# Performance work log

Measured on AMD Instinct MI355X. Metric: run time of the kernel, lower is better.

## Reference

```python
import jax, jax.numpy as jnp
import numpy as np

B, T, D_IN, D, KS = 8, 2048, 64, 512, 3
N_LAYERS = 6
TOP_P = 0.25


def _causal_conv(x, w, b, dil):
    # x: [B, C_in, T], w: [C_out, C_in, K] -> [B, C_out, T]
    pad = (w.shape[-1] - 1) * dil
    y = jax.lax.conv_general_dilated(
        x, w, window_strides=(1,), padding=[(pad, 0)], rhs_dilation=(dil,),
        dimension_numbers=('NCH', 'OIH', 'NCH'))
    return y + b[None, :, None]


def setup_inputs() -> dict:
    key = jax.random.key(0)
    ks = jax.random.split(key, 20)
    s = 0.02
    inp = {
        'x': jax.random.normal(ks[0], (B, T, D_IN), jnp.float32),
        # block 0 (d_in=64 -> d_model=512, dilation 1) + 1x1 residual
        'c1w0': jax.random.normal(ks[1], (D, D_IN, KS), jnp.float32) * s,
        'c1b0': jnp.zeros((D,), jnp.float32),
        'c2w0': jax.random.normal(ks[2], (D, D, KS), jnp.float32) * s,
        'c2b0': jnp.zeros((D,), jnp.float32),
        'resw': jax.random.normal(ks[3], (D, D_IN, 1), jnp.float32) * s,
        'resb': jnp.zeros((D,), jnp.float32),
        # blocks 1..5 stacked (512 -> 512, dilations 2,4,8,16,32), identity residual
        'c1w': jax.random.normal(ks[4], (N_LAYERS - 1, D, D, KS), jnp.float32) * s,
        'c1b': jnp.zeros((N_LAYERS - 1, D), jnp.float32),
        'c2w': jax.random.normal(ks[5], (N_LAYERS - 1, D, D, KS), jnp.float32) * s,
        'c2b': jnp.zeros((N_LAYERS - 1, D), jnp.float32),
        # attention projections (torch Linear: y = x @ W.T + b, W [out,in])
        'wq': jax.random.normal(ks[6], (D, D), jnp.float32) * s,
        'bq': jnp.zeros((D,), jnp.float32),
        'wk': jax.random.normal(ks[7], (D, D), jnp.float32) * s,
        'bk': jnp.zeros((D,), jnp.float32),
        'wv': jax.random.normal(ks[8], (D, D), jnp.float32) * s,
        'bv': jnp.zeros((D,), jnp.float32),
        'wp': jax.random.normal(ks[9], (D, D), jnp.float32) * s,
        'bp': jnp.zeros((D,), jnp.float32),
    }
    return inp


def _forward(x, c1w0, c1b0, c2w0, c2b0, resw, resb, c1w, c1b, c2w, c2b,
             wq, bq, wk, bk, wv, bv, wp, bp):
    gelu = lambda t: jax.nn.gelu(t, approximate=False)
    h = jnp.swapaxes(x, 1, 2)  # [B, D_IN, T]
    # block 0 with 1x1-conv residual (d_in != d_out)
    y = gelu(_causal_conv(h, c1w0, c1b0, 1))
    y = gelu(_causal_conv(y, c2w0, c2b0, 1))
    h = y + _causal_conv(h, resw, resb, 1)
    # blocks 1..5, identity residual
    for i in range(N_LAYERS - 1):
        dil = 2 ** (i + 1)
        y = gelu(_causal_conv(h, c1w[i], c1b[i], dil))
        y = gelu(_causal_conv(y, c2w[i], c2b[i], dil))
        h = y + h
    z = jnp.swapaxes(h, 1, 2)  # [B, T, D]

    # sparse top-p attention
    q = z @ wq.T + bq
    k = z @ wk.T + bk
    v = z @ wv.T + bv
    scores = jnp.einsum('bqd,bkd->bqk', q, k) / jnp.sqrt(jnp.float32(D))
    k_keep = max(1, int(TOP_P * T))
    vals, idx = jax.lax.top_k(scores, k_keep)  # [B, T, k_keep]
    neg_inf = jnp.array(-jnp.inf, scores.dtype)
    mask = jnp.full_like(scores, neg_inf)
    b_ix = jnp.arange(B)[:, None, None]
    t_ix = jnp.arange(T)[None, :, None]
    mask = mask.at[b_ix, t_ix, idx].set(vals)
    attn = jax.nn.softmax(mask, axis=-1)
    attn_out = jnp.einsum('bqk,bkd->bqd', attn, v)[:, -1, :]  # [B, D]

    return (z[:, -1, :] + attn_out) @ wp.T + bp


def reference(x, c1w0, c1b0, c2w0, c2b0, resw, resb, c1w, c1b, c2w, c2b,
              wq, bq, wk, bk, wv, bv, wp, bp):
    return _forward(x, c1w0, c1b0, c2w0, c2b0, resw, resb, c1w, c1b, c2w, c2b,
                    wq, bq, wk, bk, wv, bv, wp, bp)
```

## Files before the change

### kernel.cpp

```cpp
#include <hip/hip_runtime.h>
#include <hip/hip_bf16.h>
#include <math.h>

#define B_ 8
#define T_ 2048
#define PT_ 2112
#define DIN_ 64
#define D_ 512

typedef __attribute__((ext_vector_type(8))) short bf16x8;
typedef __attribute__((ext_vector_type(4))) float f32x4;

#define HROW(b, t) (((size_t)(b) * PT_ + 64 + (t)) * D_)

__device__ __forceinline__ float gelu_f(float x) {
    return 0.5f * x * (1.0f + erff(x * 0.70710678118654752440f));
}
__device__ __forceinline__ float bfu2f(unsigned short u) {
    union { float f; unsigned int i; } v; v.i = ((unsigned int)u) << 16; return v.f;
}
__device__ __forceinline__ unsigned short f2bf(float f) {
    unsigned int x = __float_as_uint(f);
    return (unsigned short)((x + 0x7FFFu + ((x >> 16) & 1u)) >> 16);
}
__device__ __forceinline__ void gload_lds16(const void* g, void* l) {
    __builtin_amdgcn_global_load_lds(
        (const __attribute__((address_space(1))) void*)g,
        (__attribute__((address_space(3))) void*)l, 16, 0, 0);
}

__global__ __launch_bounds__(256) void k_zeropad(unsigned short* xb,
                                                 unsigned short* bufA,
                                                 unsigned short* bufB) {
    const int NX = B_ * 64 * DIN_;
    const int NA = B_ * 64 * D_;
    int i = blockIdx.x * 256 + threadIdx.x;
    if (i < NX) {
        const int b = i / (64 * DIN_), r = i - b * (64 * DIN_);
        xb[(size_t)b * PT_ * DIN_ + r] = 0;
        return;
    }
    i -= NX;
    if (i < NA) {
        const int b = i / (64 * D_), r = i - b * (64 * D_);
        bufA[(size_t)b * PT_ * D_ + r] = 0;
        return;
    }
    i -= NA;
    if (i < NA) {
        const int b = i / (64 * D_), r = i - b * (64 * D_);
        bufB[(size_t)b * PT_ * D_ + r] = 0;
    }
}

__global__ __launch_bounds__(256) void k_xcvt(const float* __restrict__ x,
                                              unsigned short* __restrict__ xb, int n) {
    const int i = blockIdx.x * 256 + threadIdx.x;
    if (i >= n) return;
    const int b = i / (T_ * DIN_);
    const int r = i - b * (T_ * DIN_);
    xb[((size_t)b * PT_ + 64) * DIN_ + r] = f2bf(x[i]);
}

__global__ __launch_bounds__(256) void k_wcvt(const float* __restrict__ src,
                                              unsigned short* __restrict__ dst,
                                              int C_in, int KS) {
    const int n = 512 * C_in * KS;
    const size_t base = (size_t)blockIdx.y * n;
    for (int i = blockIdx.x * 256 + threadIdx.x; i < n; i += gridDim.x * 256) {
        const int ci = i % C_in;
        const int r = i / C_in;
        const int co = r & 511;
        const int tap = r >> 9;
        dst[base + i] = f2bf(src[base + ((size_t)co * C_in + ci) * KS + tap]);
    }
}

template <int KS, int MODE>
__global__ __launch_bounds__(256) void k_conv_mfma(const unsigned short* __restrict__ X,
                                                   const unsigned short* __restrict__ Wt,
                                                   const float* __restrict__ bias,
                                                   const unsigned short* R,
                                                   unsigned short* Y,
                                                   int C_in, int dil) {
    const int tid = threadIdx.x;
    const int t0 = blockIdx.x * 128;
    const int co0 = blockIdx.y * 128;
    const int b = blockIdx.z;
    const int back = (KS - 1) * dil;
    const int XWIN = 128 + back;

    __shared__ __align__(16) unsigned short sX[2][192 * 32];
    __shared__ __align__(16) unsigned short sW[2][KS * 128 * 32];

    const int lane = tid & 63;
    const int wv = tid >> 6;
    const int wco = (wv & 1) * 64;
    const int wt = (wv >> 1) * 64;
    const int tl = lane & 15;
    const int ch = lane >> 4;
    const int asl = ch * 8;

    f32x4 acc[4][4] = {};

    const unsigned short* Xb = X + ((size_t)b * PT_ + 64) * C_in;
    const int nxload = XWIN * 4;

    auto stage = [&](int buf, int ci0) {
        for (int i = tid; i < nxload; i += 256) {
            const int row = i >> 2, sl = i & 3;
            const int tg = t0 - back + row;
            gload_lds16(Xb + (size_t)tg * C_in + ci0 + sl * 8, &sX[buf][(i & ~63) * 8]);
        }
        for (int i = tid; i < KS * 512; i += 256) {
            const int tap = i >> 9;
            const int r = i & 511;
            const int row = r >> 2, sl = r & 3;
            gload_lds16(Wt + ((size_t)(tap * 512 + co0 + row)) * C_in + ci0 + sl * 8,
                        &sW[buf][(i & ~63) * 8]);
        }
    };

    const int NC = C_in >> 5;
    stage(0, 0);
    __syncthreads();
    int cur = 0;

    for (int c = 0; c < NC; ++c) {
        if (c + 1 < NC) stage(cur ^ 1, (c + 1) * 32);

#pragma unroll
        for (int tap = 0; tap < KS; ++tap) {
            bf16x8 a[4], bb[4];
#pragma unroll
            for (int m = 0; m < 4; ++m)
                a[m] = *reinterpret_cast<const bf16x8*>(&sW[cur][(tap * 128 + wco + m * 16 + tl) * 32 + asl]);
            const int tapoff = tap * dil;
#pragma unroll
            for (int n = 0; n < 4; ++n)
                bb[n] = *reinterpret_cast<const bf16x8*>(&sX[cur][(wt + n * 16 + tl + tapoff) * 32 + asl]);
#pragma unroll
            for (int m = 0; m < 4; ++m)
#pragma unroll
                for (int n = 0; n < 4; ++n)
                    acc[m][n] = __builtin_amdgcn_mfma_f32_16x16x32_bf16(a[m], bb[n], acc[m][n], 0, 0, 0);
        }
        __syncthreads();
        cur ^= 1;
    }

#pragma unroll
    for (int m = 0; m < 4; ++m) {
        const int co = co0 + wco + m * 16 + ch * 4;
        const float4 bv4 = *reinterpret_cast<const float4*>(&bias[co]);
#pragma unroll
        for (int n = 0; n < 4; ++n) {
            const int t = t0 + wt + n * 16 + tl;
            const size_t base = HROW(b, t) + co;
            float v[4];
            v[0] = acc[m][n][0] + bv4.x;
            v[1] = acc[m][n][1] + bv4.y;
            v[2] = acc[m][n][2] + bv4.z;
            v[3] = acc[m][n][3] + bv4.w;
            if (MODE >= 1) {
#pragma unroll
                for (int r = 0; r < 4; ++r) v[r] = gelu_f(v[r]);
            }
            if (MODE == 2) {
                const uint2 rr = *reinterpret_cast<const uint2*>(&R[base]);
                v[0] += bfu2f((unsigned short)(rr.x & 0xffffu));
                v[1] += bfu2f((unsigned short)(rr.x >> 16));
                v[2] += bfu2f((unsigned short)(rr.y & 0xffffu));
                v[3] += bfu2f((unsigned short)(rr.y >> 16));
            }
            uint2 o;
            o.x = (unsigned int)f2bf(v[0]) | ((unsigned int)f2bf(v[1]) << 16);
            o.y = (unsigned int)f2bf(v[2]) | ((unsigned int)f2bf(v[3]) << 16);
            *reinterpret_cast<uint2*>(&Y[base]) = o;
        }
    }
}

__global__ __launch_bounds__(256) void k_q(const unsigned short* __restrict__ h,
                                           const float* __restrict__ wq,
                                           const float* __restrict__ bq,
                                           float* __restrict__ q) {
    __shared__ float zs[B_ * D_];
    const int tid = threadIdx.x;
    for (int i = tid; i < B_ * D_; i += 256) {
        const int b = i >> 9, c = i & 511;
        zs[i] = bfu2f(h[HROW(b, T_ - 1) + c]);
    }
    __syncthreads();
    const int wvi = tid >> 6, lane = tid & 63;
    const int d = blockIdx.x * 4 + wvi;
    const float* wr = wq + (size_t)d * D_ + lane * 8;
    float w8[8];
#pragma unroll
    for (int j = 0; j < 8; ++j) w8[j] = wr[j];
    float acc[B_];
#pragma unroll
    for (int b = 0; b < B_; ++b) {
        float a = 0.0f;
#pragma unroll
        for (int j = 0; j < 8; ++j) a += w8[j] * zs[b * D_ + lane * 8 + j];
        acc[b] = a;
    }
#pragma unroll
    for (int off = 32; off; off >>= 1) {
#pragma unroll
        for (int b = 0; b < B_; ++b) acc[b] += __shfl_xor(acc[b], off);
    }
    if (lane == 0) {
#pragma unroll
        for (int b = 0; b < B_; ++b) q[b * D_ + d] = acc[b] + bq[d];
    }
}

__global__ __launch_bounds__(512) void k_qk(const float* __restrict__ q,
                                            const float* __restrict__ wk,
                                            const float* __restrict__ bk,
                                            float* __restrict__ qkvec,
                                            float* __restrict__ qbk) {
    const int b = blockIdx.y, dc = blockIdx.x;
    const int tid = threadIdx.x;
    __shared__ float qs[64];
    if (tid < 64) qs[tid] = q[b * D_ + dc * 64 + tid];
    __syncthreads();
    float acc = 0.0f;
    const float* wbase = wk + (size_t)(dc * 64) * D_ + tid;
#pragma unroll 8
    for (int d = 0; d < 64; ++d) acc += qs[d] * wbase[(size_t)d * D_];
    atomicAdd(&qkvec[b * D_ + tid], acc);
    if (tid < 64) {
        float p = qs[tid] * bk[dc * 64 + tid];
#pragma unroll
        for (int off = 32; off; off >>= 1) p += __shfl_xor(p, off);
        if (tid == 0) atomicAdd(&qbk[b], p);
    }
}

__global__ __launch_bounds__(256) void k_scores(const unsigned short* __restrict__ h,
                                                const float* __restrict__ qkvec,
                                                const float* __restrict__ qbk,
                                                float* __restrict__ scores) {
    const int b = blockIdx.y;
    const int tid = threadIdx.x;
    __shared__ float qs[D_];
    qs[tid] = qkvec[b * D_ + tid];
    qs[tid + 256] = qkvec[b * D_ + tid + 256];
    __syncthreads();
    const int wvi = tid >> 6, lane = tid & 63;
    const int t = blockIdx.x * 4 + wvi;
    const uint4 v = *reinterpret_cast<const uint4*>(h + HROW(b, t) + lane * 8);
    const unsigned int w[4] = {v.x, v.y, v.z, v.w};
    float acc = 0.0f;
#pragma unroll
    for (int j = 0; j < 4; ++j) {
        acc += bfu2f((unsigned short)(w[j] & 0xffffu)) * qs[lane * 8 + 2 * j];
        acc += bfu2f((unsigned short)(w[j] >> 16)) * qs[lane * 8 + 2 * j + 1];
    }
    for (int off = 32; off; off >>= 1) acc += __shfl_down(acc, off);
    if (lane == 0) scores[b * T_ + t] = (acc + qbk[b]) * 0.04419417382415922f;
}

__global__ __launch_bounds__(1024) void k_topk(const float* __restrict__ scores,
                                               float* __restrict__ wts) {
    const int b = blockIdx.x;
    __shared__ float s[T_];
    __shared__ float v[T_];
    __shared__ float red[16];
    __shared__ float denom_s;
    for (int i = threadIdx.x; i < T_; i += 1024) {
        const float x = scores[b * T_ + i];
        s[i] = x; v[i] = x;
    }
    __syncthreads();
    for (unsigned kk = 2; kk <= T_; kk <<= 1) {
        for (unsigned j = kk >> 1; j > 0; j >>= 1) {
            for (unsigned i = threadIdx.x; i < T_; i += 1024) {
                const unsigned ixj = i ^ j;
                if (ixj > i) {
                    const float a = v[i], c2 = v[ixj];
                    const bool asc = ((i & kk) == 0);
                    if ((a > c2) == asc) { v[i] = c2; v[ixj] = a; }
                }
            }
            __syncthreads();
        }
    }
    const float thr = v[T_ - 512];
    const float mx = v[T_ - 1];
    float part = 0.0f;
    for (int i = threadIdx.x; i < T_; i += 1024) {
        const float x = s[i];
        if (x >= thr) part += expf(x - mx);
    }
    for (int off = 32; off; off >>= 1) part += __shfl_down(part, off);
    const int lane = threadIdx.x & 63, wv_ = threadIdx.x >> 6;
    if (lane == 0) red[wv_] = part;
    __syncthreads();
    if (threadIdx.x == 0) {
        float d = 0.0f;
        for (int i = 0; i < 16; ++i) d += red[i];
        denom_s = d;
    }
    __syncthreads();
    const float inv = 1.0f / denom_s;
    for (int i = threadIdx.x; i < T_; i += 1024) {
        const float x = s[i];
        wts[b * T_ + i] = (x >= thr) ? expf(x - mx) * inv : 0.0f;
    }
}

__global__ __launch_bounds__(256) void k_zv(const unsigned short* __restrict__ h,
                                            const float* __restrict__ wts,
                                            float* __restrict__ zvb) {
    const int b = blockIdx.y;
    const int t0 = blockIdx.x * 256;
    const int tid = threadIdx.x;
    float a0 = 0.0f, a1 = 0.0f;
    for (int t = t0; t < t0 + 256; ++t) {
        const float w = wts[b * T_ + t];
        if (w != 0.0f) {
            const unsigned int v = *reinterpret_cast<const unsigned int*>(
                h + HROW(b, t) + tid * 2);
            a0 += w * bfu2f((unsigned short)(v & 0xffffu));
            a1 += w * bfu2f((unsigned short)(v >> 16));
        }
    }
    atomicAdd(&zvb[b * D_ + tid * 2], a0);
    atomicAdd(&zvb[b * D_ + tid * 2 + 1], a1);
}

__global__ __launch_bounds__(256) void k_u(const unsigned short* __restrict__ h,
                                           const float* __restrict__ zvb,
                                           const float* __restrict__ wv,
                                           const float* __restrict__ bv,
                                           float* __restrict__ u) {
    __shared__ float zs[B_ * D_];
    const int tid = threadIdx.x;
    for (int i = tid; i < B_ * D_; i += 256) zs[i] = zvb[i];
    __syncthreads();
    const int wvi = tid >> 6, lane = tid & 63;
    const int e = blockIdx.x * 4 + wvi;
    const float* wr = wv + (size_t)e * D_ + lane * 8;
    float w8[8];
#pragma unroll
    for (int j = 0; j < 8; ++j) w8[j] = wr[j];
    float acc[B_];
#pragma unroll
    for (int b = 0; b < B_; ++b) {
        float a = 0.0f;
#pragma unroll
        for (int j = 0; j < 8; ++j) a += w8[j] * zs[b * D_ + lane * 8 + j];
        acc[b] = a;
    }
#pragma unroll
    for (int off = 32; off; off >>= 1) {
#pragma unroll
        for (int b = 0; b < B_; ++b) acc[b] += __shfl_xor(acc[b], off);
    }
    if (lane == 0) {
#pragma unroll
        for (int b = 0; b < B_; ++b)
            u[b * D_ + e] = acc[b] + bv[e] + bfu2f(h[HROW(b, T_ - 1) + e]);
    }
}

__global__ __launch_bounds__(256) void k_out(const float* __restrict__ u,
                                             const float* __restrict__ wp,
                                             const float* __restrict__ bp,
                                             float* __restrict__ out) {
    __shared__ float us[B_ * D_];
    const int tid = threadIdx.x;
    for (int i = tid; i < B_ * D_; i += 256) us[i] = u[i];
    __syncthreads();
    const int wvi = tid >> 6, lane = tid & 63;
    const int d = blockIdx.x * 4 + wvi;
    const float* wr = wp + (size_t)d * D_ + lane * 8;
    float w8[8];
#pragma unroll
    for (int j = 0; j < 8; ++j) w8[j] = wr[j];
    float acc[B_];
#pragma unroll
    for (int b = 0; b < B_; ++b) {
        float a = 0.0f;
#pragma unroll
        for (int j = 0; j < 8; ++j) a += w8[j] * us[b * D_ + lane * 8 + j];
        acc[b] = a;
    }
#pragma unroll
    for (int off = 32; off; off >>= 1) {
#pragma unroll
        for (int b = 0; b < B_; ++b) acc[b] += __shfl_xor(acc[b], off);
    }
    if (lane == 0) {
#pragma unroll
        for (int b = 0; b < B_; ++b) out[b * D_ + d] = acc[b] + bp[d];
    }
}

extern "C" void kernel_launch(void* const* d_in, const int* in_sizes, int n_in,
                              void* d_out, int out_size, void* d_ws, size_t ws_size,
                              hipStream_t stream) {
    const float* x    = (const float*)d_in[0];
    const float* c1w0 = (const float*)d_in[1];
    const float* c1b0 = (const float*)d_in[2];
    const float* c2w0 = (const float*)d_in[3];
    const float* c2b0 = (const float*)d_in[4];
    const float* resw = (const float*)d_in[5];
    const float* resb = (const float*)d_in[6];
    const float* c1w  = (const float*)d_in[7];
    const float* c1b  = (const float*)d_in[8];
    const float* c2w  = (const float*)d_in[9];
    const float* c2b  = (const float*)d_in[10];
    const float* wq   = (const float*)d_in[11];
    const float* bq   = (const float*)d_in[12];
    const float* wk   = (const float*)d_in[13];
    const float* bk   = (const float*)d_in[14];
    const float* wvp  = (const float*)d_in[15];
    const float* bv   = (const float*)d_in[16];
    const float* wp   = (const float*)d_in[17];
    const float* bp   = (const float*)d_in[18];
    float* out = (float*)d_out;

    unsigned short* ws16 = (unsigned short*)d_ws;
    unsigned short* xb   = ws16;
    unsigned short* bufA = xb + (size_t)B_ * PT_ * DIN_;
    unsigned short* bufB = bufA + (size_t)B_ * PT_ * D_;
    unsigned short* wRes = bufB + (size_t)B_ * PT_ * D_;
    unsigned short* wC10 = wRes + 512 * 64;
    unsigned short* wC20 = wC10 + 3 * 512 * 64;
    unsigned short* wC1  = wC20 + 3 * 512 * 512;
    unsigned short* wC2  = wC1 + (size_t)5 * 3 * 512 * 512;
    float* fws  = (float*)(wC2 + (size_t)5 * 3 * 512 * 512);
    float* qv    = fws;
    float* qkvec = qv + B_ * D_;
    float* qbk   = qkvec + B_ * D_;
    float* zvb   = qbk + 8;
    float* uacc  = zvb + B_ * D_;
    float* sc    = uacc + B_ * D_;
    float* wts   = sc + B_ * T_;

    k_zeropad<<<dim3((B_ * 64 * (DIN_ + 2 * D_) + 255) / 256), 256, 0, stream>>>(xb, bufA, bufB);
    k_xcvt<<<dim3((B_ * T_ * DIN_ + 255) / 256), 256, 0, stream>>>(x, xb, B_ * T_ * DIN_);
    k_wcvt<<<dim3(128, 1), 256, 0, stream>>>(resw, wRes, DIN_, 1);
    k_wcvt<<<dim3(384, 1), 256, 0, stream>>>(c1w0, wC10, DIN_, 3);
    k_wcvt<<<dim3(768, 1), 256, 0, stream>>>(c2w0, wC20, D_, 3);
    k_wcvt<<<dim3(768, 5), 256, 0, stream>>>(c1w, wC1, D_, 3);
    k_wcvt<<<dim3(768, 5), 256, 0, stream>>>(c2w, wC2, D_, 3);
    hipMemsetAsync(qkvec, 0, (2 * B_ * D_ + 8) * sizeof(float), stream);

    const dim3 cgrid(T_ / 128, D_ / 128, B_);
    k_conv_mfma<1, 0><<<cgrid, 256, 0, stream>>>(xb, wRes, resb, nullptr, bufA, DIN_, 1);
    k_conv_mfma<3, 1><<<cgrid, 256, 0, stream>>>(xb, wC10, c1b0, nullptr, bufB, DIN_, 1);
    k_conv_mfma<3, 2><<<cgrid, 256, 0, stream>>>(bufB, wC20, c2b0, bufA, bufA, D_, 1);
    for (int i = 0; i < 5; ++i) {
        const int dil = 2 << i;
        k_conv_mfma<3, 1><<<cgrid, 256, 0, stream>>>(bufA, wC1 + (size_t)i * 3 * 512 * 512,
                                                     c1b + i * D_, nullptr, bufB, D_, dil);
        k_conv_mfma<3, 2><<<cgrid, 256, 0, stream>>>(bufB, wC2 + (size_t)i * 3 * 512 * 512,
                                                     c2b + i * D_, bufA, bufA, D_, dil);
    }

    k_q<<<128, 256, 0, stream>>>(bufA, wq, bq, qv);
    k_qk<<<dim3(8, 8), 512, 0, stream>>>(qv, wk, bk, qkvec, qbk);
    k_scores<<<dim3(T_ / 4, B_), 256, 0, stream>>>(bufA, qkvec, qbk, sc);
    k_topk<<<B_, 1024, 0, stream>>>(sc, wts);
    k_zv<<<dim3(T_ / 256, B_), 256, 0, stream>>>(bufA, wts, zvb);
    k_u<<<128, 256, 0, stream>>>(bufA, zvb, wvp, bv, uacc);
    k_out<<<128, 256, 0, stream>>>(uacc, wp, bp, out);
}
```

Before: 528.6 us.

## Widen conv K-chunk to 64 with XOR-swizzled LDS and deeper async prefetch

The MFMA causal-conv kernel now stages 64 input channels per chunk instead of 32. LDS rows are XOR-swizzled to avoid bank conflicts on the bf16x8 fragment reads. Two chunks are prefetched up front, with explicit vmcnt waits and raw s_barriers so that global-to-LDS loads overlap compute with fewer synchronisations per channel. The larger LDS footprint and launch_bounds(256,1) lower occupancy. The hardcoded vmcnt counts and the fixed 6-iteration X staging loop, which clamps row indices, depend on the exact load counts and window sizes.

```diff
diff --git a/kernel.cpp b/kernel.cpp
--- a/kernel.cpp
+++ b/kernel.cpp
@@ -77,21 +77,24 @@
 }
 
 template <int KS, int MODE>
-__global__ __launch_bounds__(256) void k_conv_mfma(const unsigned short* __restrict__ X,
-                                                   const unsigned short* __restrict__ Wt,
-                                                   const float* __restrict__ bias,
-                                                   const unsigned short* R,
-                                                   unsigned short* Y,
-                                                   int C_in, int dil) {
+__global__ __launch_bounds__(256, 1) void k_conv_mfma(const unsigned short* __restrict__ X,
+                                                      const unsigned short* __restrict__ Wt,
+                                                      const float* __restrict__ bias,
+                                                      const unsigned short* R,
+                                                      unsigned short* Y,
+                                                      int C_in, int dil) {
+    constexpr int XROWS = 192;
+    constexpr int WROWS = KS * 128;
+    constexpr int WSLOTS = WROWS * 8;
+
     const int tid = threadIdx.x;
     const int t0 = blockIdx.x * 128;
     const int co0 = blockIdx.y * 128;
     const int b = blockIdx.z;
     const int back = (KS - 1) * dil;
-    const int XWIN = 128 + back;
-
-    __shared__ __align__(16) unsigned short sX[2][192 * 32];
-    __shared__ __align__(16) unsigned short sW[2][KS * 128 * 32];
+
+    __shared__ __align__(16) unsigned short sX[2][XROWS * 64];
+    __shared__ __align__(16) unsigned short sW[2][WROWS * 64];
 
     const int lane = tid & 63;
     const int wv = tid >> 6;
@@ -99,54 +102,81 @@
     const int wt = (wv >> 1) * 64;
     const int tl = lane & 15;
     const int ch = lane >> 4;
-    const int asl = ch * 8;
 
     f32x4 acc[4][4] = {};
 
     const unsigned short* Xb = X + ((size_t)b * PT_ + 64) * C_in;
-    const int nxload = XWIN * 4;
 
     auto stage = [&](int buf, int ci0) {
-        for (int i = tid; i < nxload; i += 256) {
-            const int row = i >> 2, sl = i & 3;
-            const int tg = t0 - back + row;
-            gload_lds16(Xb + (size_t)tg * C_in + ci0 + sl * 8, &sX[buf][(i & ~63) * 8]);
-        }
-        for (int i = tid; i < KS * 512; i += 256) {
-            const int tap = i >> 9;
-            const int r = i & 511;
-            const int row = r >> 2, sl = r & 3;
-            gload_lds16(Wt + ((size_t)(tap * 512 + co0 + row)) * C_in + ci0 + sl * 8,
+#pragma unroll
+        for (int k = 0; k < 6; ++k) {
+            const int i = tid + k * 256;
+            const int row = i >> 3, s = i & 7;
+            int tg = t0 - back + row;
+            if (tg >= T_) tg = T_ - 1;
+            gload_lds16(Xb + (size_t)tg * C_in + ci0 + ((s ^ (row & 7)) << 3),
+                        &sX[buf][(i & ~63) * 8]);
+        }
+#pragma unroll
+        for (int k = 0; k < WSLOTS / 256; ++k) {
+            const int i = tid + k * 256;
+            const int row = i >> 3, s = i & 7;
+            const int tap = row >> 7, rco = row & 127;
+            gload_lds16(Wt + ((size_t)(tap * 512 + co0 + rco)) * C_in + ci0 +
+                            ((s ^ (row & 7)) << 3),
                         &sW[buf][(i & ~63) * 8]);
         }
     };
 
-    const int NC = C_in >> 5;
+    const int NC = C_in >> 6;
     stage(0, 0);
-    __syncthreads();
-    int cur = 0;
+    if (NC > 1) stage(1, 64);
 
     for (int c = 0; c < NC; ++c) {
-        if (c + 1 < NC) stage(cur ^ 1, (c + 1) * 32);
-
+        if (c + 1 < NC) {
+            if constexpr (KS == 3) asm volatile("s_waitcnt vmcnt(18)" ::: "memory");
+            else                   asm volatile("s_waitcnt vmcnt(10)" ::: "memory");
+        } else {
+            asm volatile("s_waitcnt vmcnt(0)" ::: "memory");
+        }
+        __builtin_amdgcn_sched_barrier(0);
+        __builtin_amdgcn_s_barrier();
+
+        const unsigned short* bX = sX[c & 1];
+        const unsigned short* bW = sW[c & 1];
 #pragma unroll
         for (int tap = 0; tap < KS; ++tap) {
-            bf16x8 a[4], bb[4];
-#pragma unroll
-            for (int m = 0; m < 4; ++m)
-                a[m] = *reinterpret_cast<const bf16x8*>(&sW[cur][(tap * 128 + wco + m * 16 + tl) * 32 + asl]);
             const int tapoff = tap * dil;
 #pragma unroll
-            for (int n = 0; n < 4; ++n)
-                bb[n] = *reinterpret_cast<const bf16x8*>(&sX[cur][(wt + n * 16 + tl + tapoff) * 32 + asl]);
-#pragma unroll
-            for (int m = 0; m < 4; ++m)
-#pragma unroll
-                for (int n = 0; n < 4; ++n)
-                    acc[m][n] = __builtin_amdgcn_mfma_f32_16x16x32_bf16(a[m], bb[n], acc[m][n], 0, 0, 0);
-        }
-        __syncthreads();
-        cur ^= 1;
+            for (int ks = 0; ks < 2; ++ks) {
+                const int j = ks * 4 + ch;
+                bf16x8 a[4], bb[4];
+#pragma unroll
+                for (int m = 0; m < 4; ++m) {
+                    const int wr = tap * 128 + wco + m * 16 + tl;
+                    a[m] = *reinterpret_cast<const bf16x8*>(
+                        &bW[wr * 64 + ((j ^ (wr & 7)) << 3)]);
+                }
+#pragma unroll
+                for (int n = 0; n < 4; ++n) {
+                    const int xr = wt + n * 16 + tl + tapoff;
+                    bb[n] = *reinterpret_cast<const bf16x8*>(
+                        &bX[xr * 64 + ((j ^ (xr & 7)) << 3)]);
+                }
+#pragma unroll
+                for (int m = 0; m < 4; ++m)
+#pragma unroll
+                    for (int n = 0; n < 4; ++n)
+                        acc[m][n] = __builtin_amdgcn_mfma_f32_16x16x32_bf16(a[m], bb[n], acc[m][n], 0, 0, 0);
+            }
+        }
+
+        if (c + 2 < NC) {
+            asm volatile("s_waitcnt lgkmcnt(0)" ::: "memory");
+            __builtin_amdgcn_sched_barrier(0);
+            __builtin_amdgcn_s_barrier();
+            stage(c & 1, (c + 2) * 64);
+        }
     }
 
 #pragma unroll
```

After: 645.6 us. +22.1%, slower.
